# Kernel optimization log

Measured on AMD Instinct MI355X. Metric: run time of the kernel, lower is better.

Reference implementation:

```python
import jax, jax.numpy as jnp
import numpy as np

EPS = 1e-07
B, H, W_IN = 128, 32, 32
N_CAPS, K_SEC, D_SEC, P_PRIM = 4608, 2, 16, 32


def setup_inputs() -> dict:
    key = jax.random.key(0)
    ks = jax.random.split(key, 12)
    input_x = jax.random.normal(ks[0], (B, H, W_IN, 1), dtype=jnp.float32)
    labels = jax.random.randint(ks[1], (B,), 0, K_SEC)
    y = jax.nn.one_hot(labels, K_SEC, dtype=jnp.float32)
    s = 0.05
    conv1_w = jax.random.normal(ks[2], (9, 9, 1, 256), dtype=jnp.float32) * s
    conv1_b = jnp.zeros((256,), dtype=jnp.float32)
    conv2_w = jax.random.normal(ks[3], (9, 9, 256, 1024), dtype=jnp.float32) * s
    conv2_b = jnp.zeros((1024,), dtype=jnp.float32)
    w = jax.random.normal(ks[4], (1, N_CAPS, K_SEC, D_SEC, P_PRIM), dtype=jnp.float32) * s
    d1_w = jax.random.normal(ks[5], (K_SEC * D_SEC, 256), dtype=jnp.float32) * s
    d1_b = jnp.zeros((256,), dtype=jnp.float32)
    d2_w = jax.random.normal(ks[6], (256, 512), dtype=jnp.float32) * s
    d2_b = jnp.zeros((512,), dtype=jnp.float32)
    d3_w = jax.random.normal(ks[7], (512, 1024), dtype=jnp.float32) * s
    d3_b = jnp.zeros((1024,), dtype=jnp.float32)
    return {"input_x": input_x, "y": y, "conv1_w": conv1_w, "conv1_b": conv1_b,
            "conv2_w": conv2_w, "conv2_b": conv2_b, "w": w,
            "d1_w": d1_w, "d1_b": d1_b, "d2_w": d2_w, "d2_b": d2_b,
            "d3_w": d3_w, "d3_b": d3_b}


def _conv(x, k, b, strides, padding):
    y = jax.lax.conv_general_dilated(x, k, strides, padding,
                                     dimension_numbers=("NHWC", "HWIO", "NHWC"))
    return y + b


def _squash(s):
    # s: [..., D]; squash along last axis
    s_norm = jnp.linalg.norm(s, axis=-1, keepdims=True)
    return (jnp.square(s_norm) / (1.0 + jnp.square(s_norm))) * s / (s_norm + EPS)


def reference(input_x, y, conv1_w, conv1_b, conv2_w, conv2_b, w,
              d1_w, d1_b, d2_w, d2_b, d3_w, d3_b):
    # Conv stack: [B,32,32,1] -> relu conv 9x9 valid -> [B,24,24,256]
    x = jax.nn.relu(_conv(input_x, conv1_w, conv1_b, (1, 1), "VALID"))
    # primary capsule conv 9x9 stride 2 'same': -> [B,12,12,1024]
    x = _conv(x, conv2_w, conv2_b, (2, 2), "SAME")

    # Capsule formation: [B,12,12,1024] -> u [B,4608,32]
    u = x.reshape(x.shape[0], N_CAPS, P_PRIM)
    # u_hat[b,n,k,d] = sum_p w[0,n,k,d,p] * u[b,n,p]
    u_hat = jnp.einsum("nkdp,bnp->bnkd", w[0], u)  # [B,4608,K,D]

    # Dynamic routing (r iterations)
    b_logits = jnp.zeros(u_hat.shape[:3] + (1,), dtype=u_hat.dtype)  # [B,N,K,1]
    v = None
    for _ in range(3):
        c = jax.nn.softmax(b_logits, axis=-2)               # softmax over K
        s = jnp.sum(c * u_hat, axis=1, keepdims=True)       # [B,1,K,D]
        v = _squash(s)                                      # [B,1,K,D]
        agreement = jnp.sum(u_hat * v, axis=-1, keepdims=True)  # [B,N,K,1]
        b_logits = b_logits + agreement

    # Masking with one-hot labels
    mask = y[:, None, :, None]                              # [B,1,K,1]
    v_masked = mask * v                                     # [B,1,K,D]

    # Reconstruction MLP (dropouts in source are no-ops)
    v_flat = v_masked.reshape(-1, K_SEC * D_SEC)            # [B,32]
    h1 = jax.nn.relu(v_flat @ d1_w + d1_b)
    h2 = jax.nn.relu(h1 @ d2_w + d2_b)
    recon = jax.nn.sigmoid(h2 @ d3_w + d3_b)                # [B,1024]
    return v, recon
```

## Files before the change

kernel.cpp:

```cpp
#include <hip/hip_runtime.h>
#include <hip/hip_bf16.h>

typedef __attribute__((ext_vector_type(8))) short s16x8;
typedef __attribute__((ext_vector_type(4))) int   i32x4;
typedef __attribute__((ext_vector_type(4))) float f32x4;

#define NCAPS 4608
#define BATCH 128

#define GLOAD_LDS16(gp, lp)                                                   \
  __builtin_amdgcn_global_load_lds(                                           \
      (const __attribute__((address_space(1))) void*)(gp),                    \
      (__attribute__((address_space(3))) void*)(lp), 16, 0, 0)

__global__ void transpose_w_kernel(const float* __restrict__ W,
                                   __hip_bfloat16* __restrict__ Wt) {
  __shared__ float tile[64][65];
  int kt = blockIdx.x * 64;
  int ct = blockIdx.y * 64;
  for (int i = threadIdx.x; i < 64 * 64; i += 256) {
    int r = i >> 6, c = i & 63;
    tile[r][c] = W[(size_t)(kt + r) * 1024 + ct + c];
  }
  __syncthreads();
  for (int i = threadIdx.x; i < 64 * 64; i += 256) {
    int r = i >> 6, c = i & 63;
    Wt[(size_t)(ct + r) * 20736 + kt + c] = __float2bfloat16(tile[c][r]);
  }
}

__global__ void conv1_kernel(const float* __restrict__ x,
                             const float* __restrict__ w,
                             const float* __restrict__ bias,
                             __hip_bfloat16* __restrict__ outp) {
  int by = blockIdx.x;
  int b = by / 24, y = by % 24;
  __shared__ float patch[288];
  for (int i = threadIdx.x; i < 288; i += 256) {
    int r = i >> 5, c = i & 31;
    patch[i] = x[(size_t)b * 1024 + (y + r) * 32 + c];
  }
  __syncthreads();
  int co = threadIdx.x;
  float bv = bias[co];
  float acc[24];
#pragma unroll
  for (int i = 0; i < 24; i++) acc[i] = bv;
#pragma unroll
  for (int ky = 0; ky < 9; ky++) {
    float row[32];
#pragma unroll
    for (int c = 0; c < 32; c++) row[c] = patch[ky * 32 + c];
#pragma unroll
    for (int kx = 0; kx < 9; kx++) {
      float wv = w[(ky * 9 + kx) * 256 + co];
#pragma unroll
      for (int xx = 0; xx < 24; xx++) acc[xx] += row[kx + xx] * wv;
    }
  }
  size_t obase = (((size_t)b * 31 + (y + 3)) * 31 + 3) * 256 + co;
#pragma unroll
  for (int xx = 0; xx < 24; xx++)
    outp[obase + (size_t)xx * 256] = __float2bfloat16(fmaxf(acc[xx], 0.f));
}

__global__ __launch_bounds__(256)
void conv2_mfma_kernel(const __hip_bfloat16* __restrict__ Apad,
                       const __hip_bfloat16* __restrict__ Wt,
                       const float* __restrict__ bias,
                       float* __restrict__ U) {
  __shared__ __align__(16) __hip_bfloat16 As[2][128 * 64];
  __shared__ __align__(16) __hip_bfloat16 Bs[2][128 * 64];
  int l = blockIdx.x;
  int s = l >> 7;
  int w0 = l & 127;
  int xcd = w0 & 7;
  int j = w0 >> 3;
  int bm = s * 16 + xcd * 2 + (j & 1);
  int bn = j >> 1;

  int tid = threadIdx.x;
  int lane = tid & 63, w = tid >> 6;
  int seg  = lane & 7;
  int rsub = lane >> 3;
  int sseg = seg ^ rsub;

  const __hip_bfloat16* abase[4];
  const __hip_bfloat16* bbase[4];
#pragma unroll
  for (int i = 0; i < 4; i++) {
    int r = w * 32 + i * 8 + rsub;
    int m = bm * 128 + r;
    int b = m / 144, rem = m % 144;
    int oy = rem / 12, ox = rem % 12;
    abase[i] = Apad + (((size_t)(b * 31 + oy * 2)) * 31 + ox * 2) * 256 + sseg * 8;
    int n = bn * 128 + r;
    bbase[i] = Wt + (size_t)n * 20736 + sseg * 8;
  }

  f32x4 acc[4][4];
#pragma unroll
  for (int mi = 0; mi < 4; mi++)
#pragma unroll
    for (int ni = 0; ni < 4; ni++)
#pragma unroll
      for (int r = 0; r < 4; r++) acc[mi][ni][r] = 0.f;

  int wm = w >> 1, wn = w & 1;
  int lrow = lane & 15;
  int lq = lane >> 4;

  auto STAGE = [&](int buf, int ks) {
    int pos = ks >> 2, ci0 = (ks & 3) << 6;
    int ky = pos / 9, kx = pos % 9;
    size_t aoff = (size_t)(ky * 31 + kx) * 256 + ci0;
    size_t boff = (size_t)pos * 256 + ci0;
#pragma unroll
    for (int i = 0; i < 4; i++) {
      GLOAD_LDS16(abase[i] + aoff, &As[buf][(w * 32 + i * 8) * 64]);
      GLOAD_LDS16(bbase[i] + boff, &Bs[buf][(w * 32 + i * 8) * 64]);
    }
  };

  STAGE(0, 0);
  __syncthreads();
  int cur = 0;
  for (int ks = 0; ks < 324; ++ks) {
    if (ks < 323) STAGE(cur ^ 1, ks + 1);
    const __hip_bfloat16* Ac = As[cur];
    const __hip_bfloat16* Bc = Bs[cur];
#pragma unroll
    for (int ksub = 0; ksub < 2; ksub++) {
      s16x8 af[4], bf[4];
#pragma unroll
      for (int mi = 0; mi < 4; mi++) {
        int row = wm * 64 + mi * 16 + lrow;
        int c = (ksub * 4 + lq) ^ (row & 7);
        af[mi] = *(const s16x8*)(Ac + row * 64 + c * 8);
      }
#pragma unroll
      for (int ni = 0; ni < 4; ni++) {
        int row = wn * 64 + ni * 16 + lrow;
        int c = (ksub * 4 + lq) ^ (row & 7);
        bf[ni] = *(const s16x8*)(Bc + row * 64 + c * 8);
      }
#pragma unroll
      for (int mi = 0; mi < 4; mi++)
#pragma unroll
        for (int ni = 0; ni < 4; ni++)
          acc[mi][ni] = __builtin_amdgcn_mfma_f32_16x16x32_bf16(
              af[mi], bf[ni], acc[mi][ni], 0, 0, 0);
    }
    __syncthreads();
    cur ^= 1;
  }

#pragma unroll
  for (int mi = 0; mi < 4; mi++) {
    int mg = bm * 128 + wm * 64 + mi * 16 + ((lane >> 4) << 2);
#pragma unroll
    for (int ni = 0; ni < 4; ni++) {
      int ng = bn * 128 + wn * 64 + ni * 16 + (lane & 15);
      float bv = bias[ng];
#pragma unroll
      for (int r = 0; r < 4; r++)
        U[(size_t)(mg + r) * 1024 + ng] = acc[mi][ni][r] + bv;
    }
  }
}

__global__ void uhat_kernel(const float* __restrict__ u,
                            const float* __restrict__ w,
                            float* __restrict__ uhat) {
  int n = blockIdx.x;
  __shared__ float wsm[32 * 33];
  int t = threadIdx.x;
  for (int i = t; i < 1024; i += 256)
    wsm[(i >> 5) * 33 + (i & 31)] = w[(size_t)n * 1024 + i];
  __syncthreads();
  int kd = t & 31, bs = t >> 5;
  float wr[32];
#pragma unroll
  for (int p = 0; p < 32; p++) wr[p] = wsm[kd * 33 + p];
  for (int bp = 0; bp < 16; bp++) {
    int b = bp * 8 + bs;
    size_t off = ((size_t)b * NCAPS + n) * 32 + kd;
    float uval = u[off];
    float acc = 0.f;
#pragma unroll
    for (int p = 0; p < 32; p++) acc += wr[p] * __shfl(uval, p, 32);
    uhat[off] = acc;
  }
}

__global__ __launch_bounds__(512)
void routing_decoder_kernel(const float* __restrict__ uhat,
                            const float* __restrict__ y,
                            const float* __restrict__ d1_w,
                            const float* __restrict__ d1_b,
                            const float* __restrict__ d2_w,
                            const float* __restrict__ d2_b,
                            const float* __restrict__ d3_w,
                            const float* __restrict__ d3_b,
                            float* __restrict__ out) {
  int b = blockIdx.x;
  int t = threadIdx.x;
  int lane = t & 63, wid = t >> 6;
  __shared__ float vls[32];
  __shared__ float red[8][32];
  __shared__ float vms[32];
  __shared__ float h1s[256];
  __shared__ float h2s[512];
  float a1c0[9], a1c1[9];
  const float* ub = uhat + (size_t)b * NCAPS * 32;

  for (int it = 0; it < 3; ++it) {
    float part[32];
#pragma unroll
    for (int d = 0; d < 32; ++d) part[d] = 0.f;
    float v0[16], v1[16];
    if (it > 0) {
#pragma unroll
      for (int d = 0; d < 16; ++d) { v0[d] = vls[d]; v1[d] = vls[16 + d]; }
    }
#pragma unroll
    for (int i = 0; i < 9; ++i) {
      int n = t + 512 * i;
      const float* up = ub + (size_t)n * 32;
      float uh[32];
#pragma unroll
      for (int q = 0; q < 8; ++q) {
        f32x4 tmp = *(const f32x4*)(up + q * 4);
        uh[q * 4 + 0] = tmp[0]; uh[q * 4 + 1] = tmp[1];
        uh[q * 4 + 2] = tmp[2]; uh[q * 4 + 3] = tmp[3];
      }
      float c0 = 0.5f, c1 = 0.5f;
      if (it > 0) {
        float d0 = 0.f, d1 = 0.f;
#pragma unroll
        for (int d = 0; d < 16; ++d) { d0 += uh[d] * v0[d]; d1 += uh[16 + d] * v1[d]; }
        float b0, b1;
        if (it == 1) { a1c0[i] = d0; a1c1[i] = d1; b0 = d0; b1 = d1; }
        else         { b0 = a1c0[i] + d0; b1 = a1c1[i] + d1; }
        float mx = fmaxf(b0, b1);
        float e0 = __expf(b0 - mx), e1 = __expf(b1 - mx);
        float inv = 1.f / (e0 + e1);
        c0 = e0 * inv; c1 = e1 * inv;
      }
#pragma unroll
      for (int d = 0; d < 16; ++d) {
        part[d]      += c0 * uh[d];
        part[16 + d] += c1 * uh[16 + d];
      }
    }
#pragma unroll
    for (int m = 1; m < 64; m <<= 1)
#pragma unroll
      for (int d = 0; d < 32; ++d) part[d] += __shfl_xor(part[d], m, 64);
    __syncthreads();
    if (lane == 0)
#pragma unroll
      for (int d = 0; d < 32; ++d) red[wid][d] = part[d];
    __syncthreads();
    if (t < 32) {
      float sd = 0.f;
#pragma unroll
      for (int w2 = 0; w2 < 8; ++w2) sd += red[w2][t];
      float p = sd * sd;
#pragma unroll
      for (int m = 1; m < 16; m <<= 1) p += __shfl_xor(p, m, 64);
      float f = p / (1.f + p) / (sqrtf(p) + 1e-7f);
      vls[t] = sd * f;
    }
    __syncthreads();
  }

  if (t < 32) {
    float vv = vls[t];
    out[(size_t)b * 32 + t] = vv;
    vms[t] = y[b * 2 + (t >> 4)] * vv;
  }
  __syncthreads();
  if (t < 256) {
    float acc = d1_b[t];
#pragma unroll
    for (int k = 0; k < 32; ++k) acc += vms[k] * d1_w[k * 256 + t];
    h1s[t] = fmaxf(acc, 0.f);
  }
  __syncthreads();
  {
    float acc = d2_b[t];
    for (int k = 0; k < 256; ++k) acc += h1s[k] * d2_w[k * 512 + t];
    h2s[t] = fmaxf(acc, 0.f);
  }
  __syncthreads();
  float* rout = out + 4096 + (size_t)b * 1024;
#pragma unroll
  for (int jj = 0; jj < 2; ++jj) {
    int jcol = t + jj * 512;
    float acc = d3_b[jcol];
    for (int k = 0; k < 512; ++k) acc += h2s[k] * d3_w[k * 1024 + jcol];
    rout[jcol] = 1.f / (1.f + __expf(-acc));
  }
}

extern "C" void kernel_launch(void* const* d_in, const int* in_sizes, int n_in,
                              void* d_out, int out_size, void* d_ws, size_t ws_size,
                              hipStream_t stream) {
  const float* input_x = (const float*)d_in[0];
  const float* y       = (const float*)d_in[1];
  const float* conv1_w = (const float*)d_in[2];
  const float* conv1_b = (const float*)d_in[3];
  const float* conv2_w = (const float*)d_in[4];
  const float* conv2_b = (const float*)d_in[5];
  const float* w_caps  = (const float*)d_in[6];
  const float* d1_w    = (const float*)d_in[7];
  const float* d1_b    = (const float*)d_in[8];
  const float* d2_w    = (const float*)d_in[9];
  const float* d2_b    = (const float*)d_in[10];
  const float* d3_w    = (const float*)d_in[11];
  const float* d3_b    = (const float*)d_in[12];
  float* out = (float*)d_out;

  char* ws = (char*)d_ws;
  size_t apad_bytes = (size_t)128 * 31 * 31 * 256 * 2;
  __hip_bfloat16* Apad = (__hip_bfloat16*)ws; ws += (apad_bytes + 255) & ~255ull;
  __hip_bfloat16* Wt   = (__hip_bfloat16*)ws; ws += 42467328;
  float* u     = (float*)ws; ws += 75497472;
  float* uhat  = (float*)ws; ws += 75497472;

  hipMemsetAsync(Apad, 0, apad_bytes, stream);
  transpose_w_kernel<<<dim3(324, 16), 256, 0, stream>>>(conv2_w, Wt);
  conv1_kernel<<<3072, 256, 0, stream>>>(input_x, conv1_w, conv1_b, Apad);
  conv2_mfma_kernel<<<1152, 256, 0, stream>>>(Apad, Wt, conv2_b, u);
  uhat_kernel<<<NCAPS, 256, 0, stream>>>(u, w_caps, uhat);
  routing_decoder_kernel<<<128, 512, 0, stream>>>(uhat, y, d1_w, d1_b, d2_w,
                                                  d2_b, d3_w, d3_b, out);
}
```

Baseline: 1.433 ms.

## Enlarge conv2 GEMM tile to 256x128 with 512 threads and deferred-wait pipelining

The conv2 implicit-GEMM kernel now uses 256x128 output tiles computed by 8 waves, 576 blocks instead of 1152, and a new XCD-aware block mapping. The prefetch is restructured so the next stage is issued before compute, with an explicit vmcnt wait and raw barriers in place of __syncthreads. s_setprio is raised around the MFMA section. The goal is better A/B reuse per LDS load and better overlap of global loads with compute. In exchange LDS use goes up and occupancy is limited to one block per CU.

```diff
diff --git a/kernel.cpp b/kernel.cpp
--- a/kernel.cpp
+++ b/kernel.cpp
@@ -64,38 +64,40 @@
     outp[obase + (size_t)xx * 256] = __float2bfloat16(fmaxf(acc[xx], 0.f));
 }
 
-__global__ __launch_bounds__(256)
+__global__ __launch_bounds__(512, 1)
 void conv2_mfma_kernel(const __hip_bfloat16* __restrict__ Apad,
                        const __hip_bfloat16* __restrict__ Wt,
                        const float* __restrict__ bias,
                        float* __restrict__ U) {
-  __shared__ __align__(16) __hip_bfloat16 As[2][128 * 64];
+  __shared__ __align__(16) __hip_bfloat16 As[2][256 * 64];
   __shared__ __align__(16) __hip_bfloat16 Bs[2][128 * 64];
   int l = blockIdx.x;
-  int s = l >> 7;
-  int w0 = l & 127;
-  int xcd = w0 & 7;
-  int j = w0 >> 3;
-  int bm = s * 16 + xcd * 2 + (j & 1);
-  int bn = j >> 1;
+  int xcd = l & 7;
+  int j = l >> 3;
+  int bm = xcd * 9 + (j >> 3);
+  int bn = j & 7;
 
   int tid = threadIdx.x;
   int lane = tid & 63, w = tid >> 6;
-  int seg  = lane & 7;
-  int rsub = lane >> 3;
+  int wm = w & 3, wn = w >> 2;
+  int seg = lane & 7, rsub = lane >> 3;
   int sseg = seg ^ rsub;
 
   const __hip_bfloat16* abase[4];
-  const __hip_bfloat16* bbase[4];
-#pragma unroll
-  for (int i = 0; i < 4; i++) {
-    int r = w * 32 + i * 8 + rsub;
-    int m = bm * 128 + r;
+#pragma unroll
+  for (int g = 0; g < 4; ++g) {
+    int r = (w * 4 + g) * 8 + rsub;
+    int m = bm * 256 + r;
     int b = m / 144, rem = m % 144;
     int oy = rem / 12, ox = rem % 12;
-    abase[i] = Apad + (((size_t)(b * 31 + oy * 2)) * 31 + ox * 2) * 256 + sseg * 8;
+    abase[g] = Apad + (((size_t)(b * 31 + oy * 2)) * 31 + ox * 2) * 256 + sseg * 8;
+  }
+  const __hip_bfloat16* bbase[2];
+#pragma unroll
+  for (int g = 0; g < 2; ++g) {
+    int r = (w * 2 + g) * 8 + rsub;
     int n = bn * 128 + r;
-    bbase[i] = Wt + (size_t)n * 20736 + sseg * 8;
+    bbase[g] = Wt + (size_t)n * 20736 + sseg * 8;
   }
 
   f32x4 acc[4][4];
@@ -106,31 +108,35 @@
 #pragma unroll
       for (int r = 0; r < 4; r++) acc[mi][ni][r] = 0.f;
 
-  int wm = w >> 1, wn = w & 1;
   int lrow = lane & 15;
   int lq = lane >> 4;
 
-  auto STAGE = [&](int buf, int ks) {
-    int pos = ks >> 2, ci0 = (ks & 3) << 6;
+  auto STAGE = [&](int buf, int t) {
+    int pos = t >> 2, ci0 = (t & 3) << 6;
     int ky = pos / 9, kx = pos % 9;
     size_t aoff = (size_t)(ky * 31 + kx) * 256 + ci0;
     size_t boff = (size_t)pos * 256 + ci0;
 #pragma unroll
-    for (int i = 0; i < 4; i++) {
-      GLOAD_LDS16(abase[i] + aoff, &As[buf][(w * 32 + i * 8) * 64]);
-      GLOAD_LDS16(bbase[i] + boff, &Bs[buf][(w * 32 + i * 8) * 64]);
-    }
+    for (int g = 0; g < 4; ++g)
+      GLOAD_LDS16(abase[g] + aoff, &As[buf][(w * 4 + g) * 8 * 64]);
+#pragma unroll
+    for (int g = 0; g < 2; ++g)
+      GLOAD_LDS16(bbase[g] + boff, &Bs[buf][(w * 2 + g) * 8 * 64]);
   };
 
   STAGE(0, 0);
-  __syncthreads();
-  int cur = 0;
-  for (int ks = 0; ks < 324; ++ks) {
-    if (ks < 323) STAGE(cur ^ 1, ks + 1);
+  STAGE(1, 1);
+
+  for (int t = 0; t < 324; ++t) {
+    int cur = t & 1;
+    if (t < 323) asm volatile("s_waitcnt vmcnt(6)" ::: "memory");
+    else         asm volatile("s_waitcnt vmcnt(0)" ::: "memory");
+    __builtin_amdgcn_s_barrier();
     const __hip_bfloat16* Ac = As[cur];
     const __hip_bfloat16* Bc = Bs[cur];
-#pragma unroll
-    for (int ksub = 0; ksub < 2; ksub++) {
+    __builtin_amdgcn_s_setprio(1);
+#pragma unroll
+    for (int ksub = 0; ksub < 2; ++ksub) {
       s16x8 af[4], bf[4];
 #pragma unroll
       for (int mi = 0; mi < 4; mi++) {
@@ -151,13 +157,15 @@
           acc[mi][ni] = __builtin_amdgcn_mfma_f32_16x16x32_bf16(
               af[mi], bf[ni], acc[mi][ni], 0, 0, 0);
     }
-    __syncthreads();
-    cur ^= 1;
+    __builtin_amdgcn_s_setprio(0);
+    asm volatile("s_waitcnt lgkmcnt(0)" ::: "memory");
+    __builtin_amdgcn_s_barrier();
+    if (t + 2 < 324) STAGE(cur, t + 2);
   }
 
 #pragma unroll
   for (int mi = 0; mi < 4; mi++) {
-    int mg = bm * 128 + wm * 64 + mi * 16 + ((lane >> 4) << 2);
+    int mg = bm * 256 + wm * 64 + mi * 16 + ((lane >> 4) << 2);
 #pragma unroll
     for (int ni = 0; ni < 4; ni++) {
       int ng = bn * 128 + wn * 64 + ni * 16 + (lane & 15);
@@ -332,7 +340,7 @@
   hipMemsetAsync(Apad, 0, apad_bytes, stream);
   transpose_w_kernel<<<dim3(324, 16), 256, 0, stream>>>(conv2_w, Wt);
   conv1_kernel<<<3072, 256, 0, stream>>>(input_x, conv1_w, conv1_b, Apad);
-  conv2_mfma_kernel<<<1152, 256, 0, stream>>>(Apad, Wt, conv2_b, u);
+  conv2_mfma_kernel<<<576, 512, 0, stream>>>(Apad, Wt, conv2_b, u);
   uhat_kernel<<<NCAPS, 256, 0, stream>>>(u, w_caps, uhat);
   routing_decoder_kernel<<<128, 512, 0, stream>>>(uhat, y, d1_w, d1_b, d2_w,
                                                   d2_b, d3_w, d3_b, out);
```

After: 1.498 ms. 4.5% more time.

## Single-buffer conv2 LDS tiles and store u_hat as bf16

Applied to the files above, without the earlier changes.

The conv2 MFMA kernel drops its double-buffered LDS staging in favour of a single buffer, synchronising before and after each K-chunk. This halves LDS use and may raise occupancy, but it gives up the overlap of global loads with MFMA work. Separately, u_hat is stored in bf16 instead of fp32, halving the memory traffic of the uhat write and of the three routing passes that read it, at some cost in routing precision.

```diff
diff --git a/kernel.cpp b/kernel.cpp
--- a/kernel.cpp
+++ b/kernel.cpp
@@ -12,6 +12,12 @@
   __builtin_amdgcn_global_load_lds(                                           \
       (const __attribute__((address_space(1))) void*)(gp),                    \
       (__attribute__((address_space(3))) void*)(lp), 16, 0, 0)
+
+__device__ __forceinline__ float bf2f(short h) {
+  union { unsigned u; float f; } cv;
+  cv.u = ((unsigned)(unsigned short)h) << 16;
+  return cv.f;
+}
 
 __global__ void transpose_w_kernel(const float* __restrict__ W,
                                    __hip_bfloat16* __restrict__ Wt) {
@@ -69,8 +75,8 @@
                        const __hip_bfloat16* __restrict__ Wt,
                        const float* __restrict__ bias,
                        float* __restrict__ U) {
-  __shared__ __align__(16) __hip_bfloat16 As[2][128 * 64];
-  __shared__ __align__(16) __hip_bfloat16 Bs[2][128 * 64];
+  __shared__ __align__(16) __hip_bfloat16 As[128 * 64];
+  __shared__ __align__(16) __hip_bfloat16 Bs[128 * 64];
   int l = blockIdx.x;
   int s = l >> 7;
   int w0 = l & 127;
@@ -110,49 +116,42 @@
   int lrow = lane & 15;
   int lq = lane >> 4;
 
-  auto STAGE = [&](int buf, int ks) {
-    int pos = ks >> 2, ci0 = (ks & 3) << 6;
+  for (int pos = 0; pos < 81; pos++) {
     int ky = pos / 9, kx = pos % 9;
-    size_t aoff = (size_t)(ky * 31 + kx) * 256 + ci0;
-    size_t boff = (size_t)pos * 256 + ci0;
-#pragma unroll
-    for (int i = 0; i < 4; i++) {
-      GLOAD_LDS16(abase[i] + aoff, &As[buf][(w * 32 + i * 8) * 64]);
-      GLOAD_LDS16(bbase[i] + boff, &Bs[buf][(w * 32 + i * 8) * 64]);
-    }
-  };
-
-  STAGE(0, 0);
-  __syncthreads();
-  int cur = 0;
-  for (int ks = 0; ks < 324; ++ks) {
-    if (ks < 323) STAGE(cur ^ 1, ks + 1);
-    const __hip_bfloat16* Ac = As[cur];
-    const __hip_bfloat16* Bc = Bs[cur];
-#pragma unroll
-    for (int ksub = 0; ksub < 2; ksub++) {
-      s16x8 af[4], bf[4];
-#pragma unroll
-      for (int mi = 0; mi < 4; mi++) {
-        int row = wm * 64 + mi * 16 + lrow;
-        int c = (ksub * 4 + lq) ^ (row & 7);
-        af[mi] = *(const s16x8*)(Ac + row * 64 + c * 8);
-      }
-#pragma unroll
-      for (int ni = 0; ni < 4; ni++) {
-        int row = wn * 64 + ni * 16 + lrow;
-        int c = (ksub * 4 + lq) ^ (row & 7);
-        bf[ni] = *(const s16x8*)(Bc + row * 64 + c * 8);
-      }
-#pragma unroll
-      for (int mi = 0; mi < 4; mi++)
-#pragma unroll
-        for (int ni = 0; ni < 4; ni++)
-          acc[mi][ni] = __builtin_amdgcn_mfma_f32_16x16x32_bf16(
-              af[mi], bf[ni], acc[mi][ni], 0, 0, 0);
-    }
-    __syncthreads();
-    cur ^= 1;
+    size_t aoff = (size_t)(ky * 31 + kx) * 256;
+    size_t boff = (size_t)pos * 256;
+#pragma unroll
+    for (int ci0 = 0; ci0 < 256; ci0 += 64) {
+#pragma unroll
+      for (int i = 0; i < 4; i++) {
+        GLOAD_LDS16(abase[i] + aoff + ci0, &As[(w * 32 + i * 8) * 64]);
+        GLOAD_LDS16(bbase[i] + boff + ci0, &Bs[(w * 32 + i * 8) * 64]);
+      }
+      __syncthreads();
+#pragma unroll
+      for (int ksub = 0; ksub < 2; ksub++) {
+        s16x8 af[4], bf[4];
+#pragma unroll
+        for (int mi = 0; mi < 4; mi++) {
+          int row = wm * 64 + mi * 16 + lrow;
+          int c = (ksub * 4 + lq) ^ (row & 7);
+          af[mi] = *(const s16x8*)(As + row * 64 + c * 8);
+        }
+#pragma unroll
+        for (int ni = 0; ni < 4; ni++) {
+          int row = wn * 64 + ni * 16 + lrow;
+          int c = (ksub * 4 + lq) ^ (row & 7);
+          bf[ni] = *(const s16x8*)(Bs + row * 64 + c * 8);
+        }
+#pragma unroll
+        for (int mi = 0; mi < 4; mi++)
+#pragma unroll
+          for (int ni = 0; ni < 4; ni++)
+            acc[mi][ni] = __builtin_amdgcn_mfma_f32_16x16x32_bf16(
+                af[mi], bf[ni], acc[mi][ni], 0, 0, 0);
+      }
+      __syncthreads();
+    }
   }
 
 #pragma unroll
@@ -171,7 +170,7 @@
 
 __global__ void uhat_kernel(const float* __restrict__ u,
                             const float* __restrict__ w,
-                            float* __restrict__ uhat) {
+                            __hip_bfloat16* __restrict__ uhat) {
   int n = blockIdx.x;
   __shared__ float wsm[32 * 33];
   int t = threadIdx.x;
@@ -189,12 +188,12 @@
     float acc = 0.f;
 #pragma unroll
     for (int p = 0; p < 32; p++) acc += wr[p] * __shfl(uval, p, 32);
-    uhat[off] = acc;
+    uhat[off] = __float2bfloat16(acc);
   }
 }
 
 __global__ __launch_bounds__(512)
-void routing_decoder_kernel(const float* __restrict__ uhat,
+void routing_decoder_kernel(const __hip_bfloat16* __restrict__ uhat,
                             const float* __restrict__ y,
                             const float* __restrict__ d1_w,
                             const float* __restrict__ d1_b,
@@ -212,7 +211,7 @@
   __shared__ float h1s[256];
   __shared__ float h2s[512];
   float a1c0[9], a1c1[9];
-  const float* ub = uhat + (size_t)b * NCAPS * 32;
+  const __hip_bfloat16* ub = uhat + (size_t)b * NCAPS * 32;
 
   for (int it = 0; it < 3; ++it) {
     float part[32];
@@ -226,13 +225,13 @@
 #pragma unroll
     for (int i = 0; i < 9; ++i) {
       int n = t + 512 * i;
-      const float* up = ub + (size_t)n * 32;
+      const s16x8* up8 = (const s16x8*)(ub + (size_t)n * 32);
       float uh[32];
 #pragma unroll
-      for (int q = 0; q < 8; ++q) {
-        f32x4 tmp = *(const f32x4*)(up + q * 4);
-        uh[q * 4 + 0] = tmp[0]; uh[q * 4 + 1] = tmp[1];
-        uh[q * 4 + 2] = tmp[2]; uh[q * 4 + 3] = tmp[3];
+      for (int q = 0; q < 4; ++q) {
+        s16x8 raw = up8[q];
+#pragma unroll
+        for (int jj = 0; jj < 8; ++jj) uh[q * 8 + jj] = bf2f(raw[jj]);
       }
       float c0 = 0.5f, c1 = 0.5f;
       if (it > 0) {
@@ -326,8 +325,8 @@
   size_t apad_bytes = (size_t)128 * 31 * 31 * 256 * 2;
   __hip_bfloat16* Apad = (__hip_bfloat16*)ws; ws += (apad_bytes + 255) & ~255ull;
   __hip_bfloat16* Wt   = (__hip_bfloat16*)ws; ws += 42467328;
-  float* u     = (float*)ws; ws += 75497472;
-  float* uhat  = (float*)ws; ws += 75497472;
+  float* u             = (float*)ws;          ws += 75497472;
+  __hip_bfloat16* uhat = (__hip_bfloat16*)ws; ws += 37748736;
 
   hipMemsetAsync(Apad, 0, apad_bytes, stream);
   transpose_w_kernel<<<dim3(324, 16), 256, 0, stream>>>(conv2_w, Wt);
```

Result: faster. 1.377 ms (-3.9%).
